# Kernel optimization log

Hardware: AMD Instinct MI355X
Metric: run time of the kernel (lower is better)

The kernel has to match this reference:

```python
import jax, jax.numpy as jnp
import numpy as np

B, D, K = 32768, 256, 1024


def setup_inputs() -> dict:
    key = jax.random.key(0)
    k1, k2 = jax.random.split(key)
    embedding = jax.random.normal(k1, (B, D), dtype=jnp.float32)
    codebook = jax.random.normal(k2, (K, D), dtype=jnp.float32)
    return {"embedding": embedding, "codebook": codebook}


def reference(embedding, codebook):
    # code_norms: (K,) squared L2 norm of each code
    code_norms = jnp.sum(codebook ** 2, axis=1)            # (K,)
    dots = embedding @ codebook.T                           # (B, K)
    alpha = dots / code_norms[None, :]                      # (B, K)
    # error for projecting e onto line of code c:
    #   ||e - alpha c||^2 = ||e||^2 - dots^2 / ||c||^2
    # (identical math to materializing (B,K,D) diff, without the blowup)
    e_norms = jnp.sum(embedding ** 2, axis=1, keepdims=True)  # (B, 1)
    errors = e_norms - dots ** 2 / code_norms[None, :]        # (B, K)
    indices = jnp.argmin(errors, axis=1)                      # (B,)
    # gather chosen projection: alpha[b, idx[b]] * codebook[idx[b]]
    alpha_sel = jnp.take_along_axis(alpha, indices[:, None], axis=1)  # (B, 1)
    z_out = alpha_sel * codebook[indices]                     # (B, D)
    return (z_out, indices)
```

## Files before the change

### kernel.cpp

```cpp
#include <hip/hip_runtime.h>
#include <cstdint>

#define B_ROWS 32768
#define DIM    256
#define KCODES 1024
#define NSPLIT 2

typedef _Float16 f16x8 __attribute__((ext_vector_type(8)));
typedef float    f32x4 __attribute__((ext_vector_type(4)));


__global__ __launch_bounds__(64) void vq_prep(const float* __restrict__ cb,
                                              _Float16* __restrict__ hi,
                                              _Float16* __restrict__ lo,
                                              float* __restrict__ inv_norm) {
  const int k = blockIdx.x;
  const int lane = threadIdx.x;
  float4 c = reinterpret_cast<const float4*>(cb)[k * 64 + lane];
  float nrm = c.x * c.x + c.y * c.y + c.z * c.z + c.w * c.w;
#pragma unroll
  for (int off = 32; off; off >>= 1) nrm += __shfl_xor(nrm, off);
  if (lane == 0) inv_norm[k] = 1.0f / nrm;

  float f[4] = {c.x, c.y, c.z, c.w};
  _Float16 h[4], l[4];
#pragma unroll
  for (int i = 0; i < 4; ++i) {
    h[i] = (_Float16)f[i];
    l[i] = (_Float16)((f[i] - (float)h[i]) * 2048.0f);
  }
  const int phys = (lane >> 1) ^ (k & 15);
  const int byteoff = k * 512 + phys * 16 + (lane & 1) * 8;
  *reinterpret_cast<uint2*>((char*)hi + byteoff) = *reinterpret_cast<uint2*>(h);
  *reinterpret_cast<uint2*>((char*)lo + byteoff) = *reinterpret_cast<uint2*>(l);
}

__device__ __forceinline__ void gld16(const void* g, void* l) {
  __builtin_amdgcn_global_load_lds(
      (const __attribute__((address_space(1))) uint32_t*)g,
      (__attribute__((address_space(3))) uint32_t*)l, 16, 0, 0);
}

__global__ __launch_bounds__(256, 2) void vq_main(const float* __restrict__ emb,
                                                  const _Float16* __restrict__ cbh,
                                                  const _Float16* __restrict__ cbl,
                                                  const float* __restrict__ inv_g,
                                                  float2* __restrict__ cand) {
  __shared__ uint4 Btile[4][1024];
  __shared__ float inv_s[KCODES];

  const int flat = threadIdx.x;
  const int wave = flat >> 6;
  const int lane = flat & 63;
  const int quad = lane >> 4;
  const int lr   = lane & 15;

  const int b = blockIdx.x;
  const int rowblk = ((b >> 4) << 3) | (b & 7);
  const int split  = (b >> 3) & 1;
  const int t0 = split * 32;
  const int tend = t0 + 32;

  reinterpret_cast<float4*>(inv_s)[flat] = reinterpret_cast<const float4*>(inv_g)[flat];

  f16x8 Ah[2][8], Al[2][8];
  const int row0 = rowblk * 128 + wave * 32;
#pragma unroll
  for (int s = 0; s < 2; ++s) {
    const float* rp = emb + (size_t)(row0 + s * 16 + lr) * DIM;
#pragma unroll
    for (int c = 0; c < 8; ++c) {
      const float* p = rp + c * 32 + quad * 8;
      float4 f0 = *reinterpret_cast<const float4*>(p);
      float4 f1 = *reinterpret_cast<const float4*>(p + 4);
      float f[8] = {f0.x, f0.y, f0.z, f0.w, f1.x, f1.y, f1.z, f1.w};
      f16x8 h, l;
#pragma unroll
      for (int j = 0; j < 8; ++j) {
        _Float16 hv = (_Float16)f[j];
        h[j] = hv;
        l[j] = (_Float16)((f[j] - (float)hv) * 2048.0f);
      }
      Ah[s][c] = h;
      Al[s][c] = l;
    }
  }

  __syncthreads();

  auto stage = [&](int t) {
    const char* srcH = (const char*)cbh + t * 8192;
    const char* srcL = (const char*)cbl + t * 8192;
    char* dst = (char*)&Btile[t & 3][0];
    const int off = flat * 16;
    gld16(srcH + off,        dst + off);
    gld16(srcH + 4096 + off, dst + 4096 + off);
    gld16(srcL + off,        dst + 8192 + off);
    gld16(srcL + 4096 + off, dst + 12288 + off);
  };
  stage(t0);
  stage(t0 + 1);
  stage(t0 + 2);

  float bg[2][4], bd[2][4];
  int   bk[2][4];
#pragma unroll
  for (int s = 0; s < 2; ++s)
#pragma unroll
    for (int r = 0; r < 4; ++r) { bg[s][r] = -1.0f; bd[s][r] = 0.0f; bk[s][r] = t0 * 16; }

  for (int t = t0; t < tend; ++t) {
    const int rem = tend - t;
    if (rem >= 3)      asm volatile("s_waitcnt vmcnt(8)" ::: "memory");
    else if (rem == 2) asm volatile("s_waitcnt vmcnt(4)" ::: "memory");
    else               asm volatile("s_waitcnt vmcnt(0)" ::: "memory");
    __builtin_amdgcn_s_barrier();
    __builtin_amdgcn_sched_barrier(0);

    if (rem > 3) stage(t + 3);

    const char* buf = (const char*)&Btile[t & 3][0];

    f32x4 accA0 = {0, 0, 0, 0}, accB0 = {0, 0, 0, 0};
    f32x4 accA1 = {0, 0, 0, 0}, accB1 = {0, 0, 0, 0};
    __builtin_amdgcn_s_setprio(1);
#pragma unroll
    for (int c = 0; c < 8; ++c) {
      const int g = (((c * 4 + quad) ^ lr) * 16) + lr * 512;
      f16x8 bh = *reinterpret_cast<const f16x8*>(buf + g);
      f16x8 bl = *reinterpret_cast<const f16x8*>(buf + 8192 + g);
      accA0 = __builtin_amdgcn_mfma_f32_16x16x32_f16(Ah[0][c], bh, accA0, 0, 0, 0);
      accA1 = __builtin_amdgcn_mfma_f32_16x16x32_f16(Ah[1][c], bh, accA1, 0, 0, 0);
      accB0 = __builtin_amdgcn_mfma_f32_16x16x32_f16(Al[0][c], bh, accB0, 0, 0, 0);
      accB1 = __builtin_amdgcn_mfma_f32_16x16x32_f16(Al[1][c], bh, accB1, 0, 0, 0);
      accB0 = __builtin_amdgcn_mfma_f32_16x16x32_f16(Ah[0][c], bl, accB0, 0, 0, 0);
      accB1 = __builtin_amdgcn_mfma_f32_16x16x32_f16(Ah[1][c], bl, accB1, 0, 0, 0);
    }
    __builtin_amdgcn_s_setprio(0);

    const int n = t * 16 + lr;
    const float inl = inv_s[n];
#pragma unroll
    for (int r = 0; r < 4; ++r) {
      float d0 = accA0[r] + accB0[r] * 4.8828125e-4f;
      float g0 = d0 * d0 * inl;
      if (g0 > bg[0][r]) { bg[0][r] = g0; bd[0][r] = d0; bk[0][r] = n; }
      float d1 = accA1[r] + accB1[r] * 4.8828125e-4f;
      float g1 = d1 * d1 * inl;
      if (g1 > bg[1][r]) { bg[1][r] = g1; bd[1][r] = d1; bk[1][r] = n; }
    }
  }

#pragma unroll
  for (int s = 0; s < 2; ++s) {
#pragma unroll
    for (int r = 0; r < 4; ++r) {
      float g = bg[s][r]; int k = bk[s][r]; float d = bd[s][r];
#pragma unroll
      for (int m = 1; m < 16; m <<= 1) {
        float g2 = __shfl_xor(g, m);
        int   k2 = __shfl_xor(k, m);
        float d2 = __shfl_xor(d, m);
        if (g2 > g || (g2 == g && k2 < k)) { g = g2; k = k2; d = d2; }
      }
      if (lr == 0) {
        const int row = row0 + s * 16 + quad * 4 + r;
        cand[(size_t)split * B_ROWS + row] = make_float2(d, __int_as_float(k));
      }
    }
  }
}

__global__ __launch_bounds__(256) void vq_reduce(const float2* __restrict__ cand,
                                                 const float* __restrict__ inv_g,
                                                 const float* __restrict__ cb,
                                                 float* __restrict__ out) {
  const int wave = threadIdx.x >> 6;
  const int lane = threadIdx.x & 63;
  const int row = blockIdx.x * 4 + wave;

  float best_g = -1.0f, best_d = 0.0f;
  int best_k = 0;
#pragma unroll
  for (int s = 0; s < NSPLIT; ++s) {
    float2 c = cand[(size_t)s * B_ROWS + row];
    int k = __float_as_int(c.y);
    float g = c.x * c.x * inv_g[k];
    if (g > best_g || (g == best_g && k < best_k)) {
      best_g = g; best_d = c.x; best_k = k;
    }
  }
  const float alpha = best_d * inv_g[best_k];
  float4 c4 = reinterpret_cast<const float4*>(cb)[best_k * 64 + lane];
  float4 z = {alpha * c4.x, alpha * c4.y, alpha * c4.z, alpha * c4.w};
  reinterpret_cast<float4*>(out)[(size_t)row * 64 + lane] = z;
  if (lane == 0) out[(size_t)B_ROWS * DIM + row] = (float)best_k;
}

extern "C" void kernel_launch(void* const* d_in, const int* in_sizes, int n_in,
                              void* d_out, int out_size, void* d_ws, size_t ws_size,
                              hipStream_t stream) {
  const float* emb = (const float*)d_in[0];
  const float* cb  = (const float*)d_in[1];
  _Float16* cbh = (_Float16*)d_ws;
  _Float16* cbl = (_Float16*)((char*)d_ws + (512 << 10));
  float*    inv = (float*)((char*)d_ws + (1 << 20));
  float2*   cand = (float2*)((char*)d_ws + (1 << 20) + 4096);

  vq_prep<<<KCODES, 64, 0, stream>>>(cb, cbh, cbl, inv);
  vq_main<<<(B_ROWS / 128) * NSPLIT, 256, 0, stream>>>(emb, cbh, cbl, inv, cand);
  vq_reduce<<<B_ROWS / 4, 256, 0, stream>>>(cand, inv, cb, (float*)d_out);
}
```

Measured before the change: 138.2 us.

## Split MFMA loop into two phases with batched LDS reads and extra barriers

The 8-step inner MFMA loop becomes two 4-step phases. Each phase first issues all LDS reads for its half, then hits a workgroup barrier and an lgkmcnt wait before running its MFMAs at raised priority. The correction accumulator is split in two (aBa and aBb) to break the serial dependency chain between MFMAs, and the prefetch stage is moved after the first batch of LDS reads. The aim is to overlap LDS latency and global-to-LDS traffic with matrix work and to stagger waves. In exchange it adds two extra barriers per tile and more register pressure.

```diff
diff --git a/kernel.cpp b/kernel.cpp
--- a/kernel.cpp
+++ b/kernel.cpp
@@ -40,6 +40,8 @@
       (const __attribute__((address_space(1))) uint32_t*)g,
       (__attribute__((address_space(3))) uint32_t*)l, 16, 0, 0);
 }
+
+#define MFMA16(a, b, acc) __builtin_amdgcn_mfma_f32_16x16x32_f16((a), (b), (acc), 0, 0, 0)
 
 __global__ __launch_bounds__(256, 2) void vq_main(const float* __restrict__ emb,
                                                   const _Float16* __restrict__ cbh,
@@ -114,38 +116,77 @@
     if (rem >= 3)      asm volatile("s_waitcnt vmcnt(8)" ::: "memory");
     else if (rem == 2) asm volatile("s_waitcnt vmcnt(4)" ::: "memory");
     else               asm volatile("s_waitcnt vmcnt(0)" ::: "memory");
+    __builtin_amdgcn_sched_barrier(0);
     __builtin_amdgcn_s_barrier();
     __builtin_amdgcn_sched_barrier(0);
 
-    if (rem > 3) stage(t + 3);
-
     const char* buf = (const char*)&Btile[t & 3][0];
 
-    f32x4 accA0 = {0, 0, 0, 0}, accB0 = {0, 0, 0, 0};
-    f32x4 accA1 = {0, 0, 0, 0}, accB1 = {0, 0, 0, 0};
-    __builtin_amdgcn_s_setprio(1);
-#pragma unroll
-    for (int c = 0; c < 8; ++c) {
-      const int g = (((c * 4 + quad) ^ lr) * 16) + lr * 512;
-      f16x8 bh = *reinterpret_cast<const f16x8*>(buf + g);
-      f16x8 bl = *reinterpret_cast<const f16x8*>(buf + 8192 + g);
-      accA0 = __builtin_amdgcn_mfma_f32_16x16x32_f16(Ah[0][c], bh, accA0, 0, 0, 0);
-      accA1 = __builtin_amdgcn_mfma_f32_16x16x32_f16(Ah[1][c], bh, accA1, 0, 0, 0);
-      accB0 = __builtin_amdgcn_mfma_f32_16x16x32_f16(Al[0][c], bh, accB0, 0, 0, 0);
-      accB1 = __builtin_amdgcn_mfma_f32_16x16x32_f16(Al[1][c], bh, accB1, 0, 0, 0);
-      accB0 = __builtin_amdgcn_mfma_f32_16x16x32_f16(Ah[0][c], bl, accB0, 0, 0, 0);
-      accB1 = __builtin_amdgcn_mfma_f32_16x16x32_f16(Ah[1][c], bl, accB1, 0, 0, 0);
-    }
-    __builtin_amdgcn_s_setprio(0);
+    f32x4 aA0  = {0, 0, 0, 0}, aA1  = {0, 0, 0, 0};
+    f32x4 aBa0 = {0, 0, 0, 0}, aBa1 = {0, 0, 0, 0};
+    f32x4 aBb0 = {0, 0, 0, 0}, aBb1 = {0, 0, 0, 0};
+
+    {
+      f16x8 bh[4], bl[4];
+#pragma unroll
+      for (int c = 0; c < 4; ++c) {
+        const int g = (((c * 4 + quad) ^ lr) * 16) + lr * 512;
+        bh[c] = *reinterpret_cast<const f16x8*>(buf + g);
+        bl[c] = *reinterpret_cast<const f16x8*>(buf + 8192 + g);
+      }
+      if (rem > 3) stage(t + 3);
+      __builtin_amdgcn_sched_barrier(0);
+      __builtin_amdgcn_s_barrier();
+      asm volatile("s_waitcnt lgkmcnt(0)" ::: "memory");
+      __builtin_amdgcn_sched_barrier(0);
+      __builtin_amdgcn_s_setprio(1);
+#pragma unroll
+      for (int c = 0; c < 4; ++c) {
+        aA0  = MFMA16(Ah[0][c], bh[c], aA0);
+        aA1  = MFMA16(Ah[1][c], bh[c], aA1);
+        aBa0 = MFMA16(Al[0][c], bh[c], aBa0);
+        aBa1 = MFMA16(Al[1][c], bh[c], aBa1);
+        aBb0 = MFMA16(Ah[0][c], bl[c], aBb0);
+        aBb1 = MFMA16(Ah[1][c], bl[c], aBb1);
+      }
+      __builtin_amdgcn_s_setprio(0);
+      __builtin_amdgcn_sched_barrier(0);
+    }
+
+    {
+      f16x8 bh[4], bl[4];
+#pragma unroll
+      for (int c = 0; c < 4; ++c) {
+        const int g = ((((c + 4) * 4 + quad) ^ lr) * 16) + lr * 512;
+        bh[c] = *reinterpret_cast<const f16x8*>(buf + g);
+        bl[c] = *reinterpret_cast<const f16x8*>(buf + 8192 + g);
+      }
+      __builtin_amdgcn_sched_barrier(0);
+      __builtin_amdgcn_s_barrier();
+      asm volatile("s_waitcnt lgkmcnt(0)" ::: "memory");
+      __builtin_amdgcn_sched_barrier(0);
+      __builtin_amdgcn_s_setprio(1);
+#pragma unroll
+      for (int c = 0; c < 4; ++c) {
+        aA0  = MFMA16(Ah[0][c + 4], bh[c], aA0);
+        aA1  = MFMA16(Ah[1][c + 4], bh[c], aA1);
+        aBa0 = MFMA16(Al[0][c + 4], bh[c], aBa0);
+        aBa1 = MFMA16(Al[1][c + 4], bh[c], aBa1);
+        aBb0 = MFMA16(Ah[0][c + 4], bl[c], aBb0);
+        aBb1 = MFMA16(Ah[1][c + 4], bl[c], aBb1);
+      }
+      __builtin_amdgcn_s_setprio(0);
+      __builtin_amdgcn_sched_barrier(0);
+    }
 
     const int n = t * 16 + lr;
     const float inl = inv_s[n];
 #pragma unroll
     for (int r = 0; r < 4; ++r) {
-      float d0 = accA0[r] + accB0[r] * 4.8828125e-4f;
+      float d0 = aA0[r] + (aBa0[r] + aBb0[r]) * 4.8828125e-4f;
       float g0 = d0 * d0 * inl;
       if (g0 > bg[0][r]) { bg[0][r] = g0; bd[0][r] = d0; bk[0][r] = n; }
-      float d1 = accA1[r] + accB1[r] * 4.8828125e-4f;
+      float d1 = aA1[r] + (aBa1[r] + aBb1[r]) * 4.8828125e-4f;
       float g1 = d1 * d1 * inl;
       if (g1 > bg[1][r]) { bg[1][r] = g1; bd[1][r] = d1; bk[1][r] = n; }
     }
```

After: 140.0 us. Within noise of the previous version (+1.3%).

## Load codebook fragments directly from global into registers, dropping LDS staging

Applied to the files above, without the earlier changes.

Removes the LDS ring buffer, the async global-to-LDS staging and the per-tile barriers. Each lane now reads its own B fragments and inverse norms straight from global memory (served by L2/L1), and prep writes the codebook unswizzled. It also splits the low-part accumulator into two independent chains to shorten MFMA dependencies. The risk is exposed global load latency with no explicit prefetch, plus redundant global traffic across the four waves.

```diff
diff --git a/kernel.cpp b/kernel.cpp
--- a/kernel.cpp
+++ b/kernel.cpp
@@ -29,26 +29,18 @@
     h[i] = (_Float16)f[i];
     l[i] = (_Float16)((f[i] - (float)h[i]) * 2048.0f);
   }
-  const int phys = (lane >> 1) ^ (k & 15);
-  const int byteoff = k * 512 + phys * 16 + (lane & 1) * 8;
+  const int byteoff = k * 512 + lane * 8;
   *reinterpret_cast<uint2*>((char*)hi + byteoff) = *reinterpret_cast<uint2*>(h);
   *reinterpret_cast<uint2*>((char*)lo + byteoff) = *reinterpret_cast<uint2*>(l);
 }
 
-__device__ __forceinline__ void gld16(const void* g, void* l) {
-  __builtin_amdgcn_global_load_lds(
-      (const __attribute__((address_space(1))) uint32_t*)g,
-      (__attribute__((address_space(3))) uint32_t*)l, 16, 0, 0);
-}
+#define MFMA16(a, b, acc) __builtin_amdgcn_mfma_f32_16x16x32_f16((a), (b), (acc), 0, 0, 0)
 
 __global__ __launch_bounds__(256, 2) void vq_main(const float* __restrict__ emb,
                                                   const _Float16* __restrict__ cbh,
                                                   const _Float16* __restrict__ cbl,
                                                   const float* __restrict__ inv_g,
                                                   float2* __restrict__ cand) {
-  __shared__ uint4 Btile[4][1024];
-  __shared__ float inv_s[KCODES];
-
   const int flat = threadIdx.x;
   const int wave = flat >> 6;
   const int lane = flat & 63;
@@ -60,8 +52,6 @@
   const int split  = (b >> 3) & 1;
   const int t0 = split * 32;
   const int tend = t0 + 32;
-
-  reinterpret_cast<float4*>(inv_s)[flat] = reinterpret_cast<const float4*>(inv_g)[flat];
 
   f16x8 Ah[2][8], Al[2][8];
   const int row0 = rowblk * 128 + wave * 32;
@@ -86,21 +76,9 @@
     }
   }
 
-  __syncthreads();
-
-  auto stage = [&](int t) {
-    const char* srcH = (const char*)cbh + t * 8192;
-    const char* srcL = (const char*)cbl + t * 8192;
-    char* dst = (char*)&Btile[t & 3][0];
-    const int off = flat * 16;
-    gld16(srcH + off,        dst + off);
-    gld16(srcH + 4096 + off, dst + 4096 + off);
-    gld16(srcL + off,        dst + 8192 + off);
-    gld16(srcL + 4096 + off, dst + 12288 + off);
-  };
-  stage(t0);
-  stage(t0 + 1);
-  stage(t0 + 2);
+  const char* pH = (const char*)cbh + (size_t)t0 * 8192 + lr * 512 + quad * 16;
+  const char* pL = (const char*)cbl + (size_t)t0 * 8192 + lr * 512 + quad * 16;
+  const float* pI = inv_g + t0 * 16 + lr;
 
   float bg[2][4], bd[2][4];
   int   bk[2][4];
@@ -110,45 +88,42 @@
     for (int r = 0; r < 4; ++r) { bg[s][r] = -1.0f; bd[s][r] = 0.0f; bk[s][r] = t0 * 16; }
 
   for (int t = t0; t < tend; ++t) {
-    const int rem = tend - t;
-    if (rem >= 3)      asm volatile("s_waitcnt vmcnt(8)" ::: "memory");
-    else if (rem == 2) asm volatile("s_waitcnt vmcnt(4)" ::: "memory");
-    else               asm volatile("s_waitcnt vmcnt(0)" ::: "memory");
-    __builtin_amdgcn_s_barrier();
-    __builtin_amdgcn_sched_barrier(0);
+    f16x8 bh[8], bl[8];
+#pragma unroll
+    for (int c = 0; c < 8; ++c) {
+      bh[c] = *reinterpret_cast<const f16x8*>(pH + c * 64);
+      bl[c] = *reinterpret_cast<const f16x8*>(pL + c * 64);
+    }
+    const float inl = *pI;
 
-    if (rem > 3) stage(t + 3);
+    f32x4 aA0  = {0, 0, 0, 0}, aA1  = {0, 0, 0, 0};
+    f32x4 aBa0 = {0, 0, 0, 0}, aBa1 = {0, 0, 0, 0};
+    f32x4 aBb0 = {0, 0, 0, 0}, aBb1 = {0, 0, 0, 0};
 
-    const char* buf = (const char*)&Btile[t & 3][0];
-
-    f32x4 accA0 = {0, 0, 0, 0}, accB0 = {0, 0, 0, 0};
-    f32x4 accA1 = {0, 0, 0, 0}, accB1 = {0, 0, 0, 0};
     __builtin_amdgcn_s_setprio(1);
 #pragma unroll
     for (int c = 0; c < 8; ++c) {
-      const int g = (((c * 4 + quad) ^ lr) * 16) + lr * 512;
-      f16x8 bh = *reinterpret_cast<const f16x8*>(buf + g);
-      f16x8 bl = *reinterpret_cast<const f16x8*>(buf + 8192 + g);
-      accA0 = __builtin_amdgcn_mfma_f32_16x16x32_f16(Ah[0][c], bh, accA0, 0, 0, 0);
-      accA1 = __builtin_amdgcn_mfma_f32_16x16x32_f16(Ah[1][c], bh, accA1, 0, 0, 0);
-      accB0 = __builtin_amdgcn_mfma_f32_16x16x32_f16(Al[0][c], bh, accB0, 0, 0, 0);
-      accB1 = __builtin_amdgcn_mfma_f32_16x16x32_f16(Al[1][c], bh, accB1, 0, 0, 0);
-      accB0 = __builtin_amdgcn_mfma_f32_16x16x32_f16(Ah[0][c], bl, accB0, 0, 0, 0);
-      accB1 = __builtin_amdgcn_mfma_f32_16x16x32_f16(Ah[1][c], bl, accB1, 0, 0, 0);
+      aA0  = MFMA16(Ah[0][c], bh[c], aA0);
+      aA1  = MFMA16(Ah[1][c], bh[c], aA1);
+      aBa0 = MFMA16(Al[0][c], bh[c], aBa0);
+      aBa1 = MFMA16(Al[1][c], bh[c], aBa1);
+      aBb0 = MFMA16(Ah[0][c], bl[c], aBb0);
+      aBb1 = MFMA16(Ah[1][c], bl[c], aBb1);
     }
     __builtin_amdgcn_s_setprio(0);
 
     const int n = t * 16 + lr;
-    const float inl = inv_s[n];
 #pragma unroll
     for (int r = 0; r < 4; ++r) {
-      float d0 = accA0[r] + accB0[r] * 4.8828125e-4f;
+      float d0 = aA0[r] + (aBa0[r] + aBb0[r]) * 4.8828125e-4f;
       float g0 = d0 * d0 * inl;
       if (g0 > bg[0][r]) { bg[0][r] = g0; bd[0][r] = d0; bk[0][r] = n; }
-      float d1 = accA1[r] + accB1[r] * 4.8828125e-4f;
+      float d1 = aA1[r] + (aBa1[r] + aBb1[r]) * 4.8828125e-4f;
       float g1 = d1 * d1 * inl;
       if (g1 > bg[1][r]) { bg[1][r] = g1; bd[1][r] = d1; bk[1][r] = n; }
     }
+
+    pH += 8192; pL += 8192; pI += 16;
   }
 
 #pragma unroll
```

Measured after the change: 215.2 us. 55.7% more time.
